# Kernel optimization log

Measured on AMD Instinct MI355X. Metric: run time of the kernel, lower is better.

## Reference

```python
import jax, jax.numpy as jnp
import numpy as np
from jax import lax

REPLACE_PROB = 0.12
B, I, T = 16, 256, 8192


def setup_inputs() -> dict:
    key = jax.random.key(0)
    p = REPLACE_PROB
    s = 1.0 - 2.0 * p
    # probs[p2, p1, :] = P(x_t | x_{t-2}=p2, x_{t-1}=p1); all rows [p, s, p]
    # except [2,1] which disallows jitter value 0 (the '012' triplet) and renormalizes.
    probs = np.tile(np.array([p, s, p], dtype=np.float32), (3, 3, 1))
    probs[2, 1, :] = np.array([0.0, s / (p + s), p / (p + s)], dtype=np.float32)
    x = jax.random.normal(jax.random.fold_in(key, 1), (B, I, T), dtype=jnp.float32)
    return {"x": x, "probs": jnp.asarray(probs)}


def _gen_mindex(key, probs, n_batch, n_time):
    """Sample the (n_batch, n_time+1) jitter code sequence in alphabet {0,1,2}.
    mindex[:, 0:2] = 1, mindex[:, n_time] = 1, interior sampled by a
    2nd-order Markov scan: P(x_t | x_{t-2}, x_{t-1}) = probs[p2, p1]."""
    log_probs = jnp.log(probs)  # -inf for the zeroed entry is fine for categorical

    def one_seq(k):
        ks = jax.random.split(k, n_time - 2)

        def step(carry, kk):
            p2, p1 = carry
            j = jax.random.categorical(kk, log_probs[p2, p1]).astype(jnp.int32)
            return (p1, j), j

        _, js = lax.scan(step, (jnp.int32(1), jnp.int32(1)), ks)
        return js  # (n_time - 2,)

    js = jax.vmap(one_seq)(jax.random.split(key, n_batch))  # (B, T-2)
    ones2 = jnp.ones((n_batch, 2), jnp.int32)
    ones1 = jnp.ones((n_batch, 1), jnp.int32)
    return jnp.concatenate([ones2, js, ones1], axis=1)  # (B, T+1)


def reference(x, probs):
    n_batch, n_chan, n_time = x.shape
    mindex = _gen_mindex(jax.random.key(42), probs, n_batch, n_time)
    # torch code: mindex += (arange(T+1) - 2); y[b] = index_select(x[b], 1, mindex[b, 1:])
    # => source index for output position t is (t) + (jitter - 1), jitter in {0,1,2}
    idx = mindex[:, 1:] + (jnp.arange(n_time, dtype=jnp.int32) - 1)  # (B, T), in [0, T-1]
    return jnp.take_along_axis(x, idx[:, None, :], axis=2)  # (B, I, T)
```

## Files before the change

kernel.cpp:

```cpp
#include <hip/hip_runtime.h>
#include <stdint.h>

#define T_LEN 8192
#define NSTEP 8190
#define NB 16
#define NCH 256
#define CB 4

__device__ __forceinline__ uint32_t rotl32(uint32_t v, int r) {
  return (v << r) | (v >> (32 - r));
}

__device__ __forceinline__ void tf2x32(uint32_t k0, uint32_t k1, uint32_t x0, uint32_t x1,
                                       uint32_t& o0, uint32_t& o1) {
  uint32_t ks2 = k0 ^ k1 ^ 0x1BD11BDAu;
  x0 += k0; x1 += k1;
#define RR(r) { x0 += x1; x1 = rotl32(x1, (r)); x1 ^= x0; }
  RR(13) RR(15) RR(26) RR(6)   x0 += k1;  x1 += ks2 + 1u;
  RR(17) RR(29) RR(16) RR(24)  x0 += ks2; x1 += k0 + 2u;
  RR(13) RR(15) RR(26) RR(6)   x0 += k0;  x1 += k1 + 3u;
  RR(17) RR(29) RR(16) RR(24)  x0 += k1;  x1 += ks2 + 4u;
  RR(13) RR(15) RR(26) RR(6)   x0 += ks2; x1 += k0 + 5u;
#undef RR
  o0 = x0; o1 = x1;
}

__global__ __launch_bounds__(256) void k_decide(const float* __restrict__ probs,
                                                uint8_t* __restrict__ dec) {
  int j = blockIdx.x * 256 + threadIdx.x;
  int b = blockIdx.y;
  if (j >= NSTEP) return;

  uint32_t kb0, kb1;
  tf2x32(0u, 42u, 0u, (uint32_t)b, kb0, kb1);
  uint32_t s0, s1;
  tf2x32(kb0, kb1, 0u, (uint32_t)j, s0, s1);

  uint32_t bits[3];
  {
    uint32_t y0, y1;
    tf2x32(s0, s1, 0u, 0u, y0, y1); bits[0] = y0 ^ y1;
    tf2x32(s0, s1, 0u, 1u, y0, y1); bits[1] = y0 ^ y1;
    tf2x32(s0, s1, 0u, 2u, y0, y1); bits[2] = y0 ^ y1;
  }

  double g[3];
#pragma unroll
  for (int c = 0; c < 3; ++c) {
    uint32_t k = bits[c] >> 9;
    float u = k ? (float)k * 0x1p-23f : 1.17549435e-38f;
    g[c] = -log(-log((double)u));
  }

  double lp = log((double)probs[0]);
  double ls = log((double)probs[1]);
  double l1 = log((double)probs[2 * 9 + 1 * 3 + 1]);
  double l2 = log((double)probs[2 * 9 + 1 * 3 + 2]);

  double v0 = lp + g[0], v1 = ls + g[1], v2 = lp + g[2];
  int n = 0; double best = v0;
  if (v1 > best) { n = 1; best = v1; }
  if (v2 > best) { n = 2; }
  int sp = (l1 + g[1] >= l2 + g[2]) ? 1 : 2;

  dec[b * NSTEP + j] = (uint8_t)(n | (sp << 2));
}

__device__ __forceinline__ uint64_t compose_map(uint64_t f, uint64_t g) {
  uint64_t r = 0;
#pragma unroll
  for (int st = 0; st < 9; ++st) {
    uint32_t fs = (uint32_t)((f >> (4 * st)) & 15u);
    uint32_t gs = (uint32_t)((g >> (4 * fs)) & 15u);
    r |= ((uint64_t)gs) << (4 * st);
  }
  return r;
}

__device__ __forceinline__ uint64_t shflup64(uint64_t v, int delta) {
  int lo = __shfl_up((int)(uint32_t)v, delta, 64);
  int hi = __shfl_up((int)(uint32_t)(v >> 32), delta, 64);
  return (((uint64_t)(uint32_t)hi) << 32) | (uint32_t)lo;
}

#define IDENT_MAP 0x876543210ull

__global__ __launch_bounds__(256) void k_scan(const uint8_t* __restrict__ dec,
                                              uint8_t* __restrict__ dbuf) {
  int b = blockIdx.x;
  int tid = threadIdx.x;
  int lane = tid & 63, wave = tid >> 6;
  int begin = tid * 32;
  const uint8_t* row = dec + b * NSTEP;

  uint64_t M = IDENT_MAP;
#pragma unroll
  for (int t = 0; t < 32; ++t) {
    int step = begin + t;
    if (step < NSTEP) {
      int d = row[step];
      uint32_t n = d & 3u, s = (d >> 2) & 3u;
      uint64_t Mn = 0;
#pragma unroll
      for (int st = 0; st < 9; ++st) {
        uint32_t u = (uint32_t)((M >> (4 * st)) & 15u);
        uint32_t div3 = (u * 11u) >> 5;
        uint32_t p1 = u - 3u * div3;
        uint32_t jj = (u == 7u) ? s : n;
        Mn |= ((uint64_t)(p1 * 3u + jj)) << (4 * st);
      }
      M = Mn;
    }
  }

  uint64_t I = M;
#pragma unroll
  for (int off = 1; off < 64; off <<= 1) {
    uint64_t Mp = shflup64(I, off);
    uint64_t c = compose_map(Mp, I);
    I = (lane >= off) ? c : I;
  }

  __shared__ uint64_t wmap[4];
  if (lane == 63) wmap[wave] = I;
  __syncthreads();

  uint64_t W = IDENT_MAP;
  for (int w = 0; w < wave; ++w) W = compose_map(W, wmap[w]);
  uint64_t E = shflup64(I, 1);
  if (lane == 0) E = IDENT_MAP;
  uint64_t X = compose_map(W, E);

  int state = (int)((X >> (4 * 4)) & 15u);

  uint8_t* orow = dbuf + b * T_LEN;
#pragma unroll
  for (int t = 0; t < 32; ++t) {
    int step = begin + t;
    if (step < NSTEP) {
      int d = row[step];
      uint32_t n = d & 3u, s = (d >> 2) & 3u;
      uint32_t jj = (state == 7) ? s : n;
      uint32_t div3 = ((uint32_t)state * 11u) >> 5;
      uint32_t p1 = (uint32_t)state - 3u * div3;
      state = (int)(p1 * 3u + jj);
      orow[step + 1] = (uint8_t)jj;
    }
  }
  if (tid == 0) { orow[0] = 1; orow[T_LEN - 1] = 1; }
}

__global__ __launch_bounds__(256) void k_gather(const float* __restrict__ x,
                                                const uint8_t* __restrict__ dbuf,
                                                float* __restrict__ out) {
  int b = blockIdx.z;
  int i0 = blockIdx.y * CB;
  int tid = threadIdx.x;
  int lane = tid & 63;
  int t0 = (blockIdx.x * 256 + tid) * 4;

  const uchar4 du = *(const uchar4*)(dbuf + b * T_LEN + t0);
  const int d0 = du.x, d1 = du.y, d2 = du.z, d3 = du.w;

#pragma unroll
  for (int c = 0; c < CB; ++c) {
    const float* __restrict__ xr = x + ((size_t)(b * NCH + i0 + c)) * T_LEN;
    float4 v = *(const float4*)(xr + t0);
    float left  = __shfl_up(v.w, 1);
    float right = __shfl_down(v.x, 1);
    if (lane == 0)  left  = (t0 > 0) ? xr[t0 - 1] : 0.0f;
    if (lane == 63) right = (t0 + 4 < T_LEN) ? xr[t0 + 4] : 0.0f;

    float4 o;
    o.x = (d0 == 0) ? left : ((d0 == 1) ? v.x : v.y);
    o.y = (d1 == 0) ? v.x  : ((d1 == 1) ? v.y : v.z);
    o.z = (d2 == 0) ? v.y  : ((d2 == 1) ? v.z : v.w);
    o.w = (d3 == 0) ? v.z  : ((d3 == 1) ? v.w : right);
    *(float4*)(out + ((size_t)(b * NCH + i0 + c)) * T_LEN + t0) = o;
  }
}

extern "C" void kernel_launch(void* const* d_in, const int* in_sizes, int n_in,
                              void* d_out, int out_size, void* d_ws, size_t ws_size,
                              hipStream_t stream) {
  const float* x = (const float*)d_in[0];
  const float* probs = (const float*)d_in[1];
  float* out = (float*)d_out;

  uint8_t* dec = (uint8_t*)d_ws;
  uint8_t* dbuf = (uint8_t*)d_ws + 131072;

  dim3 g1((NSTEP + 255) / 256, NB);
  k_decide<<<g1, 256, 0, stream>>>(probs, dec);

  k_scan<<<NB, 256, 0, stream>>>(dec, dbuf);

  dim3 g3(T_LEN / (256 * 4), NCH / CB, NB);
  k_gather<<<g3, 256, 0, stream>>>(x, dbuf, out);
}
```

Before: 67.82 us.

## Restructure gather to one row per block with LDS halo and nontemporal stores

```diff
diff --git a/kernel.cpp b/kernel.cpp
--- a/kernel.cpp
+++ b/kernel.cpp
@@ -5,7 +5,6 @@
 #define NSTEP 8190
 #define NB 16
 #define NCH 256
-#define CB 4
 
 __device__ __forceinline__ uint32_t rotl32(uint32_t v, int r) {
   return (v << r) | (v >> (32 - r));
@@ -150,34 +149,43 @@
   if (tid == 0) { orow[0] = 1; orow[T_LEN - 1] = 1; }
 }
 
+typedef float f32x4 __attribute__((ext_vector_type(4)));
+
 __global__ __launch_bounds__(256) void k_gather(const float* __restrict__ x,
                                                 const uint8_t* __restrict__ dbuf,
                                                 float* __restrict__ out) {
-  int b = blockIdx.z;
-  int i0 = blockIdx.y * CB;
-  int tid = threadIdx.x;
-  int lane = tid & 63;
-  int t0 = (blockIdx.x * 256 + tid) * 4;
+  __shared__ float shx[256];
+  __shared__ float shw[256];
+
+  const int bid = blockIdx.x;
+  const int tc = bid & 7;
+  const int i  = (bid >> 3) & 255;
+  const int b  = bid >> 11;
+  const int tid = threadIdx.x;
+  const int t0 = tc * 1024 + tid * 4;
 
   const uchar4 du = *(const uchar4*)(dbuf + b * T_LEN + t0);
-  const int d0 = du.x, d1 = du.y, d2 = du.z, d3 = du.w;
-
-#pragma unroll
-  for (int c = 0; c < CB; ++c) {
-    const float* __restrict__ xr = x + ((size_t)(b * NCH + i0 + c)) * T_LEN;
-    float4 v = *(const float4*)(xr + t0);
-    float left  = __shfl_up(v.w, 1);
-    float right = __shfl_down(v.x, 1);
-    if (lane == 0)  left  = (t0 > 0) ? xr[t0 - 1] : 0.0f;
-    if (lane == 63) right = (t0 + 4 < T_LEN) ? xr[t0 + 4] : 0.0f;
-
-    float4 o;
-    o.x = (d0 == 0) ? left : ((d0 == 1) ? v.x : v.y);
-    o.y = (d1 == 0) ? v.x  : ((d1 == 1) ? v.y : v.z);
-    o.z = (d2 == 0) ? v.y  : ((d2 == 1) ? v.z : v.w);
-    o.w = (d3 == 0) ? v.z  : ((d3 == 1) ? v.w : right);
-    *(float4*)(out + ((size_t)(b * NCH + i0 + c)) * T_LEN + t0) = o;
-  }
+  const float* __restrict__ xr = x + ((size_t)(b * NCH + i)) * T_LEN;
+
+  float4 v = *(const float4*)(xr + t0);
+
+  float Le = 0.0f, Re = 0.0f;
+  if (tid == 0)   Le = (t0 > 0) ? xr[t0 - 1] : 0.0f;
+  if (tid == 255) Re = (t0 + 4 < T_LEN) ? xr[t0 + 4] : 0.0f;
+
+  shx[tid] = v.x;
+  shw[tid] = v.w;
+  __syncthreads();
+
+  const float L = (tid == 0)   ? Le : shw[tid - 1];
+  const float R = (tid == 255) ? Re : shx[tid + 1];
+
+  f32x4 o;
+  o.x = (du.x == 0) ? L   : ((du.x == 1) ? v.x : v.y);
+  o.y = (du.y == 0) ? v.x : ((du.y == 1) ? v.y : v.z);
+  o.z = (du.z == 0) ? v.y : ((du.z == 1) ? v.z : v.w);
+  o.w = (du.w == 0) ? v.z : ((du.w == 1) ? v.w : R);
+  __builtin_nontemporal_store(o, (f32x4*)(out + ((size_t)(b * NCH + i)) * T_LEN + t0));
 }
 
 extern "C" void kernel_launch(void* const* d_in, const int* in_sizes, int n_in,
@@ -195,6 +203,5 @@
 
   k_scan<<<NB, 256, 0, stream>>>(dec, dbuf);
 
-  dim3 g3(T_LEN / (256 * 4), NCH / CB, NB);
-  k_gather<<<g3, 256, 0, stream>>>(x, dbuf, out);
-}
+  k_gather<<<NB * NCH * 8, 256, 0, stream>>>(x, dbuf, out);
+}
```

After: 65.18 us (median of 2 runs). -3.9%, faster.
